# Kernel tuning notes

Hardware: AMD Instinct MI355X
Metric: run time of the kernel (lower is better)

Reference implementation:

```python
import jax, jax.numpy as jnp
import numpy as np

# Sobel kernels stacked as [O=2, I=1, 3, 3]
_KX = np.array([[-1., 0., 1.], [-2., 0., 2.], [-1., 0., 1.]], dtype=np.float32)
_KY = np.array([[1., 2., 1.], [0., 0., 0.], [-1., -2., -1.]], dtype=np.float32)
_SOBEL_W = jnp.asarray(np.stack([_KX, _KY])[:, None, :, :])  # [2,1,3,3]


def _sobel(x):
    # x: [B,1,H,W] -> |Gx| + |Gy| : [B,1,H,W]
    g = jax.lax.conv_general_dilated(
        x, _SOBEL_W, window_strides=(1, 1), padding=((1, 1), (1, 1)),
        dimension_numbers=('NCHW', 'OIHW', 'NCHW'))  # [B,2,H,W]
    return jnp.sum(jnp.abs(g), axis=1, keepdims=True)


def _threshold_mask(g, k):
    # g: [B,1,H,W]; k-th SMALLEST over flattened (C*H*W) per batch (torch.kthvalue)
    B, N, H, W = g.shape
    flat = g.reshape(B, N, H * W)
    kth = jnp.sort(flat, axis=-1)[:, :, k - 1:k]  # [B,N,1]
    mask = (flat >= kth).astype(g.dtype)
    return mask.reshape(B, N, H, W)


def setup_inputs() -> dict:
    key = jax.random.key(0)
    kA, kB, kF = jax.random.split(key, 3)
    shape = (8, 3, 1024, 1024)
    return {
        'image_A': jax.random.uniform(kA, shape, dtype=jnp.float32),
        'image_B': jax.random.uniform(kB, shape, dtype=jnp.float32),
        'image_fused': jax.random.uniform(kF, shape, dtype=jnp.float32),
        'thresholds': 524288,
    }


def reference(image_A, image_B, image_fused, thresholds):
    gA = _sobel(image_A[:, :1])
    gB = _sobel(image_B[:, :1])
    gF = _sobel(image_fused[:, :1])
    joint_max = jnp.maximum(gA, gB)  # max over concat([gA,gB], dim=1) with 1 ch each
    maskA = _threshold_mask(gA, thresholds)
    maskB = _threshold_mask(gB, thresholds)
    loss = jnp.mean(jnp.abs(gF - joint_max))
    return (loss, maskA, maskB)
```

## Files before the change

kernel.cpp:

```cpp
#include <hip/hip_runtime.h>

#define IMG_H 1024
#define IMG_W 1024
#define NBATCH 8
#define NCH 3
#define NPIX (IMG_H * IMG_W)
#define SEGS 64
#define NTOT (8388608LL)

#define BINS1 4096
#define SH1 19

#define WS_MISC_OFF   0
#define WS_MISC_BYTES 4096
#define WS_H1R_OFF    (WS_MISC_OFF + WS_MISC_BYTES)
#define WS_H1R_BYTES  (2 * NBATCH * BINS1 * 4)
#define WS_H1P_OFF    (WS_H1R_OFF + WS_H1R_BYTES)
#define WS_H1P_BYTES  (2 * NBATCH * SEGS * BINS1 * 2)
#define WS_LIST_OFF   (WS_H1P_OFF + WS_H1P_BYTES)

struct Row3f { float l, c, r; };

__device__ __forceinline__ Row3f load3(const float* __restrict__ img, int y, int x) {
    Row3f o;
    if ((unsigned)y >= (unsigned)IMG_H) { o.l = o.c = o.r = 0.0f; return o; }
    const float* row = img + (size_t)y * IMG_W;
    o.c = row[x];
    o.l = (x > 0)         ? row[x - 1] : 0.0f;
    o.r = (x < IMG_W - 1) ? row[x + 1] : 0.0f;
    return o;
}

__device__ __forceinline__ float sobel_g(const Row3f& r0, const Row3f& r1, const Row3f& r2) {
    float gx = r0.r - r0.l;
    gx -= 2.0f * r1.l;
    gx += 2.0f * r1.r;
    gx -= r2.l;
    gx += r2.r;
    float gy = r0.l + 2.0f * r0.c;
    gy += r0.r;
    gy -= r2.l;
    gy -= 2.0f * r2.c;
    gy -= r2.r;
    return fabsf(gx) + fabsf(gy);
}

extern "C" __global__ __launch_bounds__(512)
void k_pass0(const float* __restrict__ A, const float* __restrict__ B,
             const float* __restrict__ F,
             unsigned short* __restrict__ hist1p, double* __restrict__ lossAcc)
{
    __shared__ unsigned int h[4 * BINS1];
    __shared__ double lsum[8];
    const int t = threadIdx.x;
    for (int i = t; i < 4 * BINS1; i += 512) h[i] = 0u;
    __syncthreads();

    const int blk = blockIdx.x;
    const int batch = blk >> 6;
    const int seg = blk & 63;
    const int y0 = (seg >> 1) * 32;
    const int x  = (seg & 1) * 512 + t;
    unsigned int* hc = h + (t >> 8) * (2 * BINS1);

    const float* a = A + (size_t)batch * NCH * NPIX;
    const float* b = B + (size_t)batch * NCH * NPIX;
    const float* f = F + (size_t)batch * NCH * NPIX;

    Row3f a0 = load3(a, y0 - 1, x), a1 = load3(a, y0, x), a2;
    Row3f b0 = load3(b, y0 - 1, x), b1 = load3(b, y0, x), b2;
    Row3f f0 = load3(f, y0 - 1, x), f1 = load3(f, y0, x), f2;

    double loss = 0.0;
    for (int i = 0; i < 32; ++i) {
        const int y = y0 + i;
        a2 = load3(a, y + 1, x);
        b2 = load3(b, y + 1, x);
        f2 = load3(f, y + 1, x);
        const float gA = sobel_g(a0, a1, a2);
        const float gB = sobel_g(b0, b1, b2);
        const float gF = sobel_g(f0, f1, f2);
        atomicAdd(&hc[__float_as_uint(gA) >> SH1], 1u);
        atomicAdd(&hc[BINS1 + (__float_as_uint(gB) >> SH1)], 1u);
        loss += (double)fabsf(gF - fmaxf(gA, gB));
        a0 = a1; a1 = a2;
        b0 = b1; b1 = b2;
        f0 = f1; f1 = f2;
    }
    __syncthreads();

    unsigned short* oA = hist1p + ((size_t)batch            * SEGS + seg) * BINS1;
    unsigned short* oB = hist1p + ((size_t)(NBATCH + batch) * SEGS + seg) * BINS1;
    for (int i = t; i < 2 * BINS1; i += 512) {
        const unsigned v = h[i] + h[2 * BINS1 + i];
        if (i < BINS1) oA[i] = (unsigned short)v;
        else           oB[i - BINS1] = (unsigned short)v;
    }

    for (int off = 32; off > 0; off >>= 1) loss += __shfl_down(loss, off);
    if ((t & 63) == 0) lsum[t >> 6] = loss;
    __syncthreads();
    if (t == 0) {
        double s = 0.0;
        for (int i = 0; i < 8; ++i) s += lsum[i];
        atomicAdd(lossAcc, s);
    }
}

extern "C" __global__ __launch_bounds__(256)
void k_scan1a(const unsigned short* __restrict__ hist1p, unsigned int* __restrict__ hist1r)
{
    const int idx = blockIdx.x * 256 + threadIdx.x;
    const int ib  = idx >> 12;
    const int bin = idx & (BINS1 - 1);
    const unsigned short* p = hist1p + (size_t)ib * SEGS * BINS1 + bin;
    unsigned int s = 0;
    #pragma unroll 8
    for (int sg = 0; sg < SEGS; ++sg) s += p[(size_t)sg * BINS1];
    hist1r[idx] = s;
}

extern "C" __global__ __launch_bounds__(1024)
void k_scan1b(const unsigned int* __restrict__ hist1r, const int* __restrict__ kptr,
              int* __restrict__ sel1, int* __restrict__ resid1)
{
    const int ib = blockIdx.x, t = threadIdx.x;
    const unsigned int* hr = hist1r + (size_t)ib * BINS1;
    long long kl = (long long)kptr[0];
    if (kl < 1 || kl > (long long)NPIX) {
        float kf = ((const float*)kptr)[0];
        kl = (long long)kf;
        if (kl < 1) kl = 1;
        if (kl > NPIX) kl = NPIX;
    }
    const unsigned k = (unsigned)kl;

    const uint4 c = ((const uint4*)hr)[t];
    const unsigned s = c.x + c.y + c.z + c.w;
    __shared__ unsigned ls[1024];
    ls[t] = s; __syncthreads();
    for (int off = 1; off < 1024; off <<= 1) {
        unsigned v = (t >= off) ? ls[t - off] : 0u;
        __syncthreads();
        ls[t] += v;
        __syncthreads();
    }
    const unsigned incl = ls[t];
    const unsigned excl = incl - s;
    if (excl < k && k <= incl) {
        unsigned cum = excl; int bin = t * 4;
        if (cum + c.x < k) { cum += c.x; ++bin;
          if (cum + c.y < k) { cum += c.y; ++bin;
            if (cum + c.z < k) { cum += c.z; ++bin; } } }
        sel1[ib] = bin;
        resid1[ib] = (int)(k - cum);
    }
}

#define PB_ROWS 32
extern "C" __global__ __launch_bounds__(1024)
void k_passB(const float* __restrict__ A, const float* __restrict__ B,
             const int* __restrict__ sel1, unsigned int* __restrict__ gCnt,
             uint2* __restrict__ list, unsigned cap, float* __restrict__ out)
{
    const int t = threadIdx.x;
    const int blk = blockIdx.x;
    const int batch = blk >> 5;
    const int y0 = (blk & 31) * PB_ROWS;
    const int x = t;

    const float* a = A + (size_t)batch * NCH * NPIX;
    const float* b = B + (size_t)batch * NCH * NPIX;
    const unsigned sA = (unsigned)sel1[batch];
    const unsigned sB = (unsigned)sel1[NBATCH + batch];
    float* mA = out + 1 + (size_t)batch * NPIX;
    float* mB = out + 1 + (size_t)NTOT + (size_t)batch * NPIX;

    __shared__ uint2 bufA[2048], bufB[2048];
    __shared__ unsigned cntA, cntB, baseA, baseB;
    if (t == 0) { cntA = 0u; cntB = 0u; }
    __syncthreads();

    Row3f a0 = load3(a, y0 - 1, x), a1 = load3(a, y0, x), a2;
    Row3f b0 = load3(b, y0 - 1, x), b1 = load3(b, y0, x), b2;
    for (int i = 0; i < PB_ROWS; ++i) {
        const int y = y0 + i;
        a2 = load3(a, y + 1, x);
        b2 = load3(b, y + 1, x);
        const unsigned uA = __float_as_uint(sobel_g(a0, a1, a2));
        const unsigned uB = __float_as_uint(sobel_g(b0, b1, b2));
        const unsigned binA = uA >> SH1, binB = uB >> SH1;
        const unsigned idx = (unsigned)y * IMG_W + (unsigned)x;
        mA[idx] = (binA > sA) ? 1.0f : 0.0f;
        mB[idx] = (binB > sB) ? 1.0f : 0.0f;
        if (binA == sA) { unsigned p = atomicAdd(&cntA, 1u); bufA[p] = make_uint2(uA, idx); }
        if (binB == sB) { unsigned p = atomicAdd(&cntB, 1u); bufB[p] = make_uint2(uB, idx); }
        a0 = a1; a1 = a2;
        b0 = b1; b1 = b2;

        __syncthreads();
        const bool last = (i == PB_ROWS - 1);
        const unsigned nA = cntA, nB = cntB;
        const bool doA = (nA >= 1024u) || (last && nA > 0u);
        const bool doB = (nB >= 1024u) || (last && nB > 0u);
        if (doA || doB) {
            if (t == 0) {
                if (doA) baseA = atomicAdd(&gCnt[batch], nA);
                if (doB) baseB = atomicAdd(&gCnt[NBATCH + batch], nB);
            }
            __syncthreads();
            if (doA) {
                const unsigned bs = baseA;
                for (unsigned j = t; j < nA; j += 1024u) {
                    const unsigned d = bs + j;
                    if (d < cap) list[(size_t)batch * cap + d] = bufA[j];
                }
            }
            if (doB) {
                const unsigned bs = baseB;
                for (unsigned j = t; j < nB; j += 1024u) {
                    const unsigned d = bs + j;
                    if (d < cap) list[(size_t)(NBATCH + batch) * cap + d] = bufB[j];
                }
            }
            __syncthreads();
            if (t == 0) { if (doA) cntA = 0u; if (doB) cntB = 0u; }
        }
        __syncthreads();
    }
}

extern "C" __global__ __launch_bounds__(1024)
void k_selectfix(const uint2* __restrict__ list, const unsigned int* __restrict__ gCnt,
                 unsigned cap, const int* __restrict__ sel1, const int* __restrict__ resid1,
                 const double* __restrict__ lossAcc, float* __restrict__ out)
{
    const int ib = blockIdx.x, t = threadIdx.x;
    const unsigned n = min(gCnt[ib], cap);
    const unsigned kk = (unsigned)resid1[ib];
    const uint2* L = list + (size_t)ib * cap;

    __shared__ unsigned h2[BINS1];
    __shared__ unsigned ls[1024];
    __shared__ unsigned bcast[4];
    if (t < 4) bcast[t] = 0u;
    for (int i = t; i < BINS1; i += 1024) h2[i] = 0u;
    __syncthreads();

    for (unsigned j = t; j < n; j += 1024u) atomicAdd(&h2[(L[j].x >> 7) & 4095u], 1u);
    __syncthreads();

    const unsigned c0 = h2[4 * t], c1 = h2[4 * t + 1], c2 = h2[4 * t + 2], c3 = h2[4 * t + 3];
    const unsigned s = c0 + c1 + c2 + c3;
    ls[t] = s; __syncthreads();
    for (int off = 1; off < 1024; off <<= 1) {
        unsigned v = (t >= off) ? ls[t - off] : 0u;
        __syncthreads();
        ls[t] += v;
        __syncthreads();
    }
    {
        const unsigned incl = ls[t], excl = incl - s;
        if (excl < kk && kk <= incl) {
            unsigned cum = excl; unsigned bin = 4u * t;
            if (cum + c0 < kk) { cum += c0; ++bin;
              if (cum + c1 < kk) { cum += c1; ++bin;
                if (cum + c2 < kk) { cum += c2; ++bin; } } }
            bcast[0] = bin;
            bcast[1] = kk - cum;
        }
    }
    __syncthreads();
    const unsigned sel2 = bcast[0], k3 = bcast[1];

    if (t < 128) h2[t] = 0u;
    __syncthreads();
    for (unsigned j = t; j < n; j += 1024u) {
        const unsigned b = L[j].x;
        if (((b >> 7) & 4095u) == sel2) atomicAdd(&h2[b & 127u], 1u);
    }
    __syncthreads();
    {
        const unsigned s3 = (t < 128) ? h2[t] : 0u;
        ls[t] = s3; __syncthreads();
        for (int off = 1; off < 1024; off <<= 1) {
            unsigned v = (t >= off) ? ls[t - off] : 0u;
            __syncthreads();
            ls[t] += v;
            __syncthreads();
        }
        const unsigned incl = ls[t], excl = incl - s3;
        if (t < 128 && excl < k3 && k3 <= incl) {
            bcast[2] = ((unsigned)sel1[ib] << SH1) | (sel2 << 7) | (unsigned)t;
        }
    }
    __syncthreads();
    const unsigned kth = bcast[2];

    float* m = out + 1 + (size_t)ib * NPIX;
    for (unsigned j = t; j < n; j += 1024u) {
        const uint2 e = L[j];
        m[e.y] = (e.x >= kth) ? 1.0f : 0.0f;
    }
    if (ib == 0 && t == 0) out[0] = (float)(lossAcc[0] * (1.0 / 8388608.0));
}

extern "C" void kernel_launch(void* const* d_in, const int* in_sizes, int n_in,
                              void* d_out, int out_size, void* d_ws, size_t ws_size,
                              hipStream_t stream)
{
    const float* A = (const float*)d_in[0];
    const float* B = (const float*)d_in[1];
    const float* F = (const float*)d_in[2];
    const int* kptr = (const int*)d_in[3];
    float* out = (float*)d_out;

    if (ws_size < (size_t)WS_LIST_OFF + 16 * 8 * 1024) return;

    char* ws = (char*)d_ws;
    double* lossAcc        = (double*)(ws + WS_MISC_OFF);
    unsigned int* gCnt     = (unsigned int*)(ws + WS_MISC_OFF + 64);
    unsigned int* hist1r   = (unsigned int*)(ws + WS_H1R_OFF);
    unsigned short* hist1p = (unsigned short*)(ws + WS_H1P_OFF);
    uint2* list            = (uint2*)(ws + WS_LIST_OFF);
    int* sel1              = (int*)(ws + WS_MISC_OFF + 128);
    int* resid1            = (int*)(ws + WS_MISC_OFF + 256);

    unsigned long long capll = (ws_size - WS_LIST_OFF) / (16ull * 8ull);
    unsigned cap = (capll > (unsigned long long)NPIX) ? (unsigned)NPIX : (unsigned)capll;

    hipMemsetAsync(ws, 0, WS_MISC_BYTES, stream);

    k_pass0    <<<dim3(NBATCH * SEGS), dim3(512), 0, stream>>>(A, B, F, hist1p, lossAcc);
    k_scan1a   <<<dim3(2 * NBATCH * BINS1 / 256), dim3(256), 0, stream>>>(hist1p, hist1r);
    k_scan1b   <<<dim3(2 * NBATCH), dim3(1024), 0, stream>>>(hist1r, kptr, sel1, resid1);
    k_passB    <<<dim3(NBATCH * 32), dim3(1024), 0, stream>>>(A, B, sel1, gCnt, list, cap, out);
    k_selectfix<<<dim3(2 * NBATCH), dim3(1024), 0, stream>>>(list, gCnt, cap, sel1, resid1, lossAcc, out);
}
```

Measured before the change: 344.8 us.

## Fuse all select passes into one cooperative kernel with grid syncs

After: 638.7 us. 85.2% more time.

```diff
diff --git a/kernel.cpp b/kernel.cpp
--- a/kernel.cpp
+++ b/kernel.cpp
@@ -1,4 +1,7 @@
 #include <hip/hip_runtime.h>
+#include <hip/hip_cooperative_groups.h>
+
+namespace cg = cooperative_groups;
 
 #define IMG_H 1024
 #define IMG_W 1024
@@ -15,9 +18,10 @@
 #define WS_MISC_BYTES 4096
 #define WS_H1R_OFF    (WS_MISC_OFF + WS_MISC_BYTES)
 #define WS_H1R_BYTES  (2 * NBATCH * BINS1 * 4)
+#define WS_LISTC_OFF  (WS_H1R_OFF + WS_H1R_BYTES)
 #define WS_H1P_OFF    (WS_H1R_OFF + WS_H1R_BYTES)
 #define WS_H1P_BYTES  (2 * NBATCH * SEGS * BINS1 * 2)
-#define WS_LIST_OFF   (WS_H1P_OFF + WS_H1P_BYTES)
+#define WS_LISTF_OFF  (WS_H1P_OFF + WS_H1P_BYTES)
 
 struct Row3f { float l, c, r; };
 
@@ -45,6 +49,239 @@
     return fabsf(gx) + fabsf(gy);
 }
 
+__device__ __forceinline__ unsigned read_k(const int* kptr) {
+    long long kl = (long long)kptr[0];
+    if (kl < 1 || kl > (long long)NPIX) {
+        float kf = ((const float*)kptr)[0];
+        kl = (long long)kf;
+        if (kl < 1) kl = 1;
+        if (kl > NPIX) kl = NPIX;
+    }
+    return (unsigned)kl;
+}
+
+union SharedU {
+    struct { unsigned h[2 * BINS1]; double lsum[8]; } a;
+    struct { uint2 bufA[1024], bufB[1024]; unsigned cnt[2], base[2]; } b;
+    struct { unsigned h2[BINS1]; unsigned ls[512]; unsigned bc[4]; } c;
+};
+
+extern "C" __global__ __launch_bounds__(512)
+void k_fused(const float* __restrict__ A, const float* __restrict__ B,
+             const float* __restrict__ F, const int* __restrict__ kptr,
+             unsigned* __restrict__ hist1r, double* __restrict__ lossAcc,
+             unsigned* __restrict__ gCnt, int* __restrict__ sel1, int* __restrict__ resid1,
+             uint2* __restrict__ list, unsigned cap, float* __restrict__ out)
+{
+    __shared__ SharedU sh;
+    cg::grid_group grid = cg::this_grid();
+    const int t = threadIdx.x;
+    const int blk = blockIdx.x;
+    const int batch = blk >> 5;
+    const int y0 = (blk & 31) * 32;
+
+    const float* a = A + (size_t)batch * NCH * NPIX;
+    const float* b = B + (size_t)batch * NCH * NPIX;
+    const float* f = F + (size_t)batch * NCH * NPIX;
+
+    for (int i = t; i < 2 * BINS1; i += 512) sh.a.h[i] = 0u;
+    __syncthreads();
+
+    double loss = 0.0;
+    for (int half = 0; half < 2; ++half) {
+        const int x = half * 512 + t;
+        Row3f a0 = load3(a, y0 - 1, x), a1 = load3(a, y0, x), a2;
+        Row3f b0 = load3(b, y0 - 1, x), b1 = load3(b, y0, x), b2;
+        Row3f f0 = load3(f, y0 - 1, x), f1 = load3(f, y0, x), f2;
+        for (int i = 0; i < 32; ++i) {
+            const int y = y0 + i;
+            a2 = load3(a, y + 1, x);
+            b2 = load3(b, y + 1, x);
+            f2 = load3(f, y + 1, x);
+            const float gA = sobel_g(a0, a1, a2);
+            const float gB = sobel_g(b0, b1, b2);
+            const float gF = sobel_g(f0, f1, f2);
+            atomicAdd(&sh.a.h[__float_as_uint(gA) >> SH1], 1u);
+            atomicAdd(&sh.a.h[BINS1 + (__float_as_uint(gB) >> SH1)], 1u);
+            loss += (double)fabsf(gF - fmaxf(gA, gB));
+            a0 = a1; a1 = a2;
+            b0 = b1; b1 = b2;
+            f0 = f1; f1 = f2;
+        }
+    }
+    __syncthreads();
+
+    for (int i = t; i < 2 * BINS1; i += 512) {
+        const unsigned v = sh.a.h[i];
+        if (v) {
+            const int ib = (i < BINS1) ? batch : (NBATCH + batch);
+            atomicAdd(&hist1r[(size_t)ib * BINS1 + (i & (BINS1 - 1))], v);
+        }
+    }
+    for (int off = 32; off > 0; off >>= 1) loss += __shfl_down(loss, off);
+    if ((t & 63) == 0) sh.a.lsum[t >> 6] = loss;
+    __syncthreads();
+    if (t == 0) {
+        double s = 0.0;
+        for (int i = 0; i < 8; ++i) s += sh.a.lsum[i];
+        atomicAdd(lossAcc, s);
+    }
+
+    grid.sync();
+
+    if (blk < 16) {
+        const unsigned k = read_k(kptr);
+        const uint4* hr4 = (const uint4*)(hist1r + (size_t)blk * BINS1);
+        const uint4 ca = hr4[2 * t], cb = hr4[2 * t + 1];
+        unsigned cc[8] = {ca.x, ca.y, ca.z, ca.w, cb.x, cb.y, cb.z, cb.w};
+        unsigned s = 0;
+        #pragma unroll
+        for (int j = 0; j < 8; ++j) s += cc[j];
+        sh.c.ls[t] = s; __syncthreads();
+        for (int off = 1; off < 512; off <<= 1) {
+            unsigned v = (t >= off) ? sh.c.ls[t - off] : 0u;
+            __syncthreads();
+            sh.c.ls[t] += v;
+            __syncthreads();
+        }
+        const unsigned incl = sh.c.ls[t], excl = incl - s;
+        if (excl < k && k <= incl) {
+            unsigned cum = excl, bin = 8u * t;
+            #pragma unroll
+            for (int j = 0; j < 8; ++j) {
+                if (cum + cc[j] < k) { cum += cc[j]; ++bin; } else break;
+            }
+            sel1[blk] = (int)bin;
+            resid1[blk] = (int)(k - cum);
+        }
+    }
+
+    grid.sync();
+
+    const unsigned sA = (unsigned)sel1[batch];
+    const unsigned sB = (unsigned)sel1[NBATCH + batch];
+    float* mA = out + 1 + (size_t)batch * NPIX;
+    float* mB = out + 1 + (size_t)NTOT + (size_t)batch * NPIX;
+
+    for (int half = 0; half < 2; ++half) {
+        const int x = half * 512 + t;
+        if (t == 0) { sh.b.cnt[0] = 0u; sh.b.cnt[1] = 0u; }
+        __syncthreads();
+        Row3f a0 = load3(a, y0 - 1, x), a1 = load3(a, y0, x), a2;
+        Row3f b0 = load3(b, y0 - 1, x), b1 = load3(b, y0, x), b2;
+        for (int i = 0; i < 32; ++i) {
+            const int y = y0 + i;
+            a2 = load3(a, y + 1, x);
+            b2 = load3(b, y + 1, x);
+            const unsigned uA = __float_as_uint(sobel_g(a0, a1, a2));
+            const unsigned uB = __float_as_uint(sobel_g(b0, b1, b2));
+            const unsigned binA = uA >> SH1, binB = uB >> SH1;
+            const unsigned idx = (unsigned)y * IMG_W + (unsigned)x;
+            mA[idx] = (binA > sA) ? 1.0f : 0.0f;
+            mB[idx] = (binB > sB) ? 1.0f : 0.0f;
+            if (binA == sA) { unsigned p = atomicAdd(&sh.b.cnt[0], 1u); if (p < 1024u) sh.b.bufA[p] = make_uint2(uA, idx); }
+            if (binB == sB) { unsigned p = atomicAdd(&sh.b.cnt[1], 1u); if (p < 1024u) sh.b.bufB[p] = make_uint2(uB, idx); }
+            a0 = a1; a1 = a2;
+            b0 = b1; b1 = b2;
+
+            if ((i & 1) == 1 || i == 31) {
+                __syncthreads();
+                const unsigned nA = sh.b.cnt[0], nB = sh.b.cnt[1];
+                if (nA | nB) {
+                    if (t == 0) {
+                        if (nA) sh.b.base[0] = atomicAdd(&gCnt[batch], nA);
+                        if (nB) sh.b.base[1] = atomicAdd(&gCnt[NBATCH + batch], nB);
+                    }
+                    __syncthreads();
+                    for (unsigned j = t; j < nA; j += 512u) {
+                        const unsigned d = sh.b.base[0] + j;
+                        if (d < cap) list[(size_t)batch * cap + d] = sh.b.bufA[j];
+                    }
+                    for (unsigned j = t; j < nB; j += 512u) {
+                        const unsigned d = sh.b.base[1] + j;
+                        if (d < cap) list[(size_t)(NBATCH + batch) * cap + d] = sh.b.bufB[j];
+                    }
+                    __syncthreads();
+                    if (t == 0) { sh.b.cnt[0] = 0u; sh.b.cnt[1] = 0u; }
+                }
+                __syncthreads();
+            }
+        }
+    }
+
+    grid.sync();
+
+    if (blk < 16) {
+        const int ib = blk;
+        const unsigned n = min(gCnt[ib], cap);
+        const unsigned kk = (unsigned)resid1[ib];
+        const uint2* L = list + (size_t)ib * cap;
+
+        if (t < 4) sh.c.bc[t] = 0u;
+        for (int i = t; i < BINS1; i += 512) sh.c.h2[i] = 0u;
+        __syncthreads();
+
+        for (unsigned j = t; j < n; j += 512u) atomicAdd(&sh.c.h2[(L[j].x >> 7) & 4095u], 1u);
+        __syncthreads();
+
+        unsigned cc[8];
+        unsigned s = 0;
+        #pragma unroll
+        for (int j = 0; j < 8; ++j) { cc[j] = sh.c.h2[8 * t + j]; s += cc[j]; }
+        sh.c.ls[t] = s; __syncthreads();
+        for (int off = 1; off < 512; off <<= 1) {
+            unsigned v = (t >= off) ? sh.c.ls[t - off] : 0u;
+            __syncthreads();
+            sh.c.ls[t] += v;
+            __syncthreads();
+        }
+        {
+            const unsigned incl = sh.c.ls[t], excl = incl - s;
+            if (excl < kk && kk <= incl) {
+                unsigned cum = excl, bin = 8u * t;
+                #pragma unroll
+                for (int j = 0; j < 8; ++j) {
+                    if (cum + cc[j] < kk) { cum += cc[j]; ++bin; } else break;
+                }
+                sh.c.bc[0] = bin;
+                sh.c.bc[1] = kk - cum;
+            }
+        }
+        __syncthreads();
+        const unsigned sel2 = sh.c.bc[0], k3 = sh.c.bc[1];
+
+        if (t < 128) sh.c.h2[t] = 0u;
+        __syncthreads();
+        for (unsigned j = t; j < n; j += 512u) {
+            const unsigned bb = L[j].x;
+            if (((bb >> 7) & 4095u) == sel2) atomicAdd(&sh.c.h2[bb & 127u], 1u);
+        }
+        __syncthreads();
+        {
+            const unsigned s3 = (t < 128) ? sh.c.h2[t] : 0u;
+            sh.c.ls[t] = s3; __syncthreads();
+            for (int off = 1; off < 512; off <<= 1) {
+                unsigned v = (t >= off) ? sh.c.ls[t - off] : 0u;
+                __syncthreads();
+                sh.c.ls[t] += v;
+                __syncthreads();
+            }
+            const unsigned incl = sh.c.ls[t], excl = incl - s3;
+            if (t < 128 && excl < k3 && k3 <= incl)
+                sh.c.bc[2] = ((unsigned)sel1[ib] << SH1) | (sel2 << 7) | (unsigned)t;
+        }
+        __syncthreads();
+        const unsigned kth = sh.c.bc[2];
+
+        float* m = out + 1 + (size_t)ib * NPIX;
+        for (unsigned j = t; j < n; j += 512u) {
+            const uint2 e = L[j];
+            m[e.y] = (e.x >= kth) ? 1.0f : 0.0f;
+        }
+        if (ib == 0 && t == 0) out[0] = (float)(lossAcc[0] * (1.0 / 8388608.0));
+    }
+}
+
 extern "C" __global__ __launch_bounds__(512)
 void k_pass0(const float* __restrict__ A, const float* __restrict__ B,
              const float* __restrict__ F,
@@ -55,22 +292,18 @@
     const int t = threadIdx.x;
     for (int i = t; i < 4 * BINS1; i += 512) h[i] = 0u;
     __syncthreads();
-
     const int blk = blockIdx.x;
     const int batch = blk >> 6;
     const int seg = blk & 63;
     const int y0 = (seg >> 1) * 32;
     const int x  = (seg & 1) * 512 + t;
     unsigned int* hc = h + (t >> 8) * (2 * BINS1);
-
     const float* a = A + (size_t)batch * NCH * NPIX;
     const float* b = B + (size_t)batch * NCH * NPIX;
     const float* f = F + (size_t)batch * NCH * NPIX;
-
     Row3f a0 = load3(a, y0 - 1, x), a1 = load3(a, y0, x), a2;
     Row3f b0 = load3(b, y0 - 1, x), b1 = load3(b, y0, x), b2;
     Row3f f0 = load3(f, y0 - 1, x), f1 = load3(f, y0, x), f2;
-
     double loss = 0.0;
     for (int i = 0; i < 32; ++i) {
         const int y = y0 + i;
@@ -83,12 +316,9 @@
         atomicAdd(&hc[__float_as_uint(gA) >> SH1], 1u);
         atomicAdd(&hc[BINS1 + (__float_as_uint(gB) >> SH1)], 1u);
         loss += (double)fabsf(gF - fmaxf(gA, gB));
-        a0 = a1; a1 = a2;
-        b0 = b1; b1 = b2;
-        f0 = f1; f1 = f2;
-    }
-    __syncthreads();
-
+        a0 = a1; a1 = a2; b0 = b1; b1 = b2; f0 = f1; f1 = f2;
+    }
+    __syncthreads();
     unsigned short* oA = hist1p + ((size_t)batch            * SEGS + seg) * BINS1;
     unsigned short* oB = hist1p + ((size_t)(NBATCH + batch) * SEGS + seg) * BINS1;
     for (int i = t; i < 2 * BINS1; i += 512) {
@@ -96,7 +326,6 @@
         if (i < BINS1) oA[i] = (unsigned short)v;
         else           oB[i - BINS1] = (unsigned short)v;
     }
-
     for (int off = 32; off > 0; off >>= 1) loss += __shfl_down(loss, off);
     if ((t & 63) == 0) lsum[t >> 6] = loss;
     __syncthreads();
@@ -117,7 +346,7 @@
     unsigned int s = 0;
     #pragma unroll 8
     for (int sg = 0; sg < SEGS; ++sg) s += p[(size_t)sg * BINS1];
-    hist1r[idx] = s;
+    atomicAdd(&hist1r[idx], s);
 }
 
 extern "C" __global__ __launch_bounds__(1024)
@@ -126,15 +355,7 @@
 {
     const int ib = blockIdx.x, t = threadIdx.x;
     const unsigned int* hr = hist1r + (size_t)ib * BINS1;
-    long long kl = (long long)kptr[0];
-    if (kl < 1 || kl > (long long)NPIX) {
-        float kf = ((const float*)kptr)[0];
-        kl = (long long)kf;
-        if (kl < 1) kl = 1;
-        if (kl > NPIX) kl = NPIX;
-    }
-    const unsigned k = (unsigned)kl;
-
+    const unsigned k = read_k(kptr);
     const uint4 c = ((const uint4*)hr)[t];
     const unsigned s = c.x + c.y + c.z + c.w;
     __shared__ unsigned ls[1024];
@@ -145,8 +366,7 @@
         ls[t] += v;
         __syncthreads();
     }
-    const unsigned incl = ls[t];
-    const unsigned excl = incl - s;
+    const unsigned incl = ls[t], excl = incl - s;
     if (excl < k && k <= incl) {
         unsigned cum = excl; int bin = t * 4;
         if (cum + c.x < k) { cum += c.x; ++bin;
@@ -168,19 +388,16 @@
     const int batch = blk >> 5;
     const int y0 = (blk & 31) * PB_ROWS;
     const int x = t;
-
     const float* a = A + (size_t)batch * NCH * NPIX;
     const float* b = B + (size_t)batch * NCH * NPIX;
     const unsigned sA = (unsigned)sel1[batch];
     const unsigned sB = (unsigned)sel1[NBATCH + batch];
     float* mA = out + 1 + (size_t)batch * NPIX;
     float* mB = out + 1 + (size_t)NTOT + (size_t)batch * NPIX;
-
     __shared__ uint2 bufA[2048], bufB[2048];
     __shared__ unsigned cntA, cntB, baseA, baseB;
     if (t == 0) { cntA = 0u; cntB = 0u; }
     __syncthreads();
-
     Row3f a0 = load3(a, y0 - 1, x), a1 = load3(a, y0, x), a2;
     Row3f b0 = load3(b, y0 - 1, x), b1 = load3(b, y0, x), b2;
     for (int i = 0; i < PB_ROWS; ++i) {
@@ -195,9 +412,7 @@
         mB[idx] = (binB > sB) ? 1.0f : 0.0f;
         if (binA == sA) { unsigned p = atomicAdd(&cntA, 1u); bufA[p] = make_uint2(uA, idx); }
         if (binB == sB) { unsigned p = atomicAdd(&cntB, 1u); bufB[p] = make_uint2(uB, idx); }
-        a0 = a1; a1 = a2;
-        b0 = b1; b1 = b2;
-
+        a0 = a1; a1 = a2; b0 = b1; b1 = b2;
         __syncthreads();
         const bool last = (i == PB_ROWS - 1);
         const unsigned nA = cntA, nB = cntB;
@@ -209,19 +424,13 @@
                 if (doB) baseB = atomicAdd(&gCnt[NBATCH + batch], nB);
             }
             __syncthreads();
-            if (doA) {
-                const unsigned bs = baseA;
-                for (unsigned j = t; j < nA; j += 1024u) {
-                    const unsigned d = bs + j;
-                    if (d < cap) list[(size_t)batch * cap + d] = bufA[j];
-                }
-            }
-            if (doB) {
-                const unsigned bs = baseB;
-                for (unsigned j = t; j < nB; j += 1024u) {
-                    const unsigned d = bs + j;
-                    if (d < cap) list[(size_t)(NBATCH + batch) * cap + d] = bufB[j];
-                }
+            if (doA) for (unsigned j = t; j < nA; j += 1024u) {
+                const unsigned d = baseA + j;
+                if (d < cap) list[(size_t)batch * cap + d] = bufA[j];
+            }
+            if (doB) for (unsigned j = t; j < nB; j += 1024u) {
+                const unsigned d = baseB + j;
+                if (d < cap) list[(size_t)(NBATCH + batch) * cap + d] = bufB[j];
             }
             __syncthreads();
             if (t == 0) { if (doA) cntA = 0u; if (doB) cntB = 0u; }
@@ -239,17 +448,14 @@
     const unsigned n = min(gCnt[ib], cap);
     const unsigned kk = (unsigned)resid1[ib];
     const uint2* L = list + (size_t)ib * cap;
-
     __shared__ unsigned h2[BINS1];
     __shared__ unsigned ls[1024];
     __shared__ unsigned bcast[4];
     if (t < 4) bcast[t] = 0u;
     for (int i = t; i < BINS1; i += 1024) h2[i] = 0u;
     __syncthreads();
-
     for (unsigned j = t; j < n; j += 1024u) atomicAdd(&h2[(L[j].x >> 7) & 4095u], 1u);
     __syncthreads();
-
     const unsigned c0 = h2[4 * t], c1 = h2[4 * t + 1], c2 = h2[4 * t + 2], c3 = h2[4 * t + 3];
     const unsigned s = c0 + c1 + c2 + c3;
     ls[t] = s; __syncthreads();
@@ -272,7 +478,6 @@
     }
     __syncthreads();
     const unsigned sel2 = bcast[0], k3 = bcast[1];
-
     if (t < 128) h2[t] = 0u;
     __syncthreads();
     for (unsigned j = t; j < n; j += 1024u) {
@@ -290,13 +495,11 @@
             __syncthreads();
         }
         const unsigned incl = ls[t], excl = incl - s3;
-        if (t < 128 && excl < k3 && k3 <= incl) {
+        if (t < 128 && excl < k3 && k3 <= incl)
             bcast[2] = ((unsigned)sel1[ib] << SH1) | (sel2 << 7) | (unsigned)t;
-        }
     }
     __syncthreads();
     const unsigned kth = bcast[2];
-
     float* m = out + 1 + (size_t)ib * NPIX;
     for (unsigned j = t; j < n; j += 1024u) {
         const uint2 e = L[j];
@@ -315,25 +518,35 @@
     const int* kptr = (const int*)d_in[3];
     float* out = (float*)d_out;
 
-    if (ws_size < (size_t)WS_LIST_OFF + 16 * 8 * 1024) return;
+    if (ws_size < (size_t)WS_LISTF_OFF + 16 * 8 * 1024) return;
 
     char* ws = (char*)d_ws;
     double* lossAcc        = (double*)(ws + WS_MISC_OFF);
     unsigned int* gCnt     = (unsigned int*)(ws + WS_MISC_OFF + 64);
-    unsigned int* hist1r   = (unsigned int*)(ws + WS_H1R_OFF);
-    unsigned short* hist1p = (unsigned short*)(ws + WS_H1P_OFF);
-    uint2* list            = (uint2*)(ws + WS_LIST_OFF);
     int* sel1              = (int*)(ws + WS_MISC_OFF + 128);
     int* resid1            = (int*)(ws + WS_MISC_OFF + 256);
-
-    unsigned long long capll = (ws_size - WS_LIST_OFF) / (16ull * 8ull);
-    unsigned cap = (capll > (unsigned long long)NPIX) ? (unsigned)NPIX : (unsigned)capll;
-
-    hipMemsetAsync(ws, 0, WS_MISC_BYTES, stream);
-
-    k_pass0    <<<dim3(NBATCH * SEGS), dim3(512), 0, stream>>>(A, B, F, hist1p, lossAcc);
-    k_scan1a   <<<dim3(2 * NBATCH * BINS1 / 256), dim3(256), 0, stream>>>(hist1p, hist1r);
-    k_scan1b   <<<dim3(2 * NBATCH), dim3(1024), 0, stream>>>(hist1r, kptr, sel1, resid1);
-    k_passB    <<<dim3(NBATCH * 32), dim3(1024), 0, stream>>>(A, B, sel1, gCnt, list, cap, out);
-    k_selectfix<<<dim3(2 * NBATCH), dim3(1024), 0, stream>>>(list, gCnt, cap, sel1, resid1, lossAcc, out);
-}
+    unsigned int* hist1r   = (unsigned int*)(ws + WS_H1R_OFF);
+    uint2* listC           = (uint2*)(ws + WS_LISTC_OFF);
+
+    unsigned long long capCll = (ws_size - WS_LISTC_OFF) / (16ull * 8ull);
+    unsigned capC = (capCll > (unsigned long long)NPIX) ? (unsigned)NPIX : (unsigned)capCll;
+
+    hipMemsetAsync(ws, 0, WS_MISC_BYTES + WS_H1R_BYTES, stream);
+
+    void* kargs[] = {(void*)&A, (void*)&B, (void*)&F, (void*)&kptr,
+                     (void*)&hist1r, (void*)&lossAcc, (void*)&gCnt,
+                     (void*)&sel1, (void*)&resid1, (void*)&listC, (void*)&capC, (void*)&out};
+    hipError_t e = hipLaunchCooperativeKernel((const void*)k_fused, dim3(256), dim3(512),
+                                              kargs, 0, stream);
+    if (e != hipSuccess) {
+        unsigned short* hist1p = (unsigned short*)(ws + WS_H1P_OFF);
+        uint2* listF           = (uint2*)(ws + WS_LISTF_OFF);
+        unsigned long long capFll = (ws_size - WS_LISTF_OFF) / (16ull * 8ull);
+        unsigned capF = (capFll > (unsigned long long)NPIX) ? (unsigned)NPIX : (unsigned)capFll;
+        k_pass0    <<<dim3(NBATCH * SEGS), dim3(512), 0, stream>>>(A, B, F, hist1p, lossAcc);
+        k_scan1a   <<<dim3(2 * NBATCH * BINS1 / 256), dim3(256), 0, stream>>>(hist1p, hist1r);
+        k_scan1b   <<<dim3(2 * NBATCH), dim3(1024), 0, stream>>>(hist1r, kptr, sel1, resid1);
+        k_passB    <<<dim3(NBATCH * 32), dim3(1024), 0, stream>>>(A, B, sel1, gCnt, listF, capF, out);
+        k_selectfix<<<dim3(2 * NBATCH), dim3(1024), 0, stream>>>(listF, gCnt, capF, sel1, resid1, lossAcc, out);
+    }
+}
```
